# Kernel tuning notes

Hardware: AMD Instinct MI355X
Metric: run time of the kernel (lower is better)

The kernel has to match this reference:

```python
import jax, jax.numpy as jnp
import numpy as np

# Master-Slave MoE: dense shared 'master' expert Mlp applied to every token,
# plus num_experts 'slave' Mlp experts combined via top-k softmax gating,
# output = master(x) + sum_k gate_k * expert_k(x). Each Mlp: fc2(gelu(fc1(x))).

DIM = 512
HID = 4 * DIM
NUM_EXPERTS = 8
TOP_K = 2


def mlp(x, w1, b1, w2, b2):
    h = jax.nn.gelu(jnp.einsum('bnd,dh->bnh', x, w1) + b1)
    return jnp.einsum('bnh,hd->bnd', h, w2) + b2


def setup_inputs() -> dict:
    key = jax.random.key(0)
    ks = jax.random.split(key, 10)
    B, N = 4, 4096
    s1 = 1.0 / np.sqrt(DIM)
    s2 = 1.0 / np.sqrt(HID)
    return {
        'x': jax.random.normal(ks[0], (B, N, DIM), jnp.float32),
        'gate_w': jax.random.normal(ks[1], (DIM, NUM_EXPERTS), jnp.float32) * s1,
        'master_w1': jax.random.normal(ks[2], (DIM, HID), jnp.float32) * s1,
        'master_b1': jnp.zeros((HID,), jnp.float32),
        'master_w2': jax.random.normal(ks[3], (HID, DIM), jnp.float32) * s2,
        'master_b2': jnp.zeros((DIM,), jnp.float32),
        'expert_w1': jax.random.normal(ks[4], (NUM_EXPERTS, DIM, HID), jnp.float32) * s1,
        'expert_b1': jnp.zeros((NUM_EXPERTS, HID), jnp.float32),
        'expert_w2': jax.random.normal(ks[5], (NUM_EXPERTS, HID, DIM), jnp.float32) * s2,
        'expert_b2': jnp.zeros((NUM_EXPERTS, DIM), jnp.float32),
    }


def reference(x, gate_w, master_w1, master_b1, master_w2, master_b2,
              expert_w1, expert_b1, expert_w2, expert_b2):
    B, N, D = x.shape
    # Router: top-k softmax gating over experts
    logits = jnp.einsum('bnd,de->bne', x, gate_w)  # [B,N,E]
    topv, topi = jax.lax.top_k(logits, TOP_K)       # [B,N,K]
    gates_k = jax.nn.softmax(topv, axis=-1)         # [B,N,K]
    # dense gate matrix [B,N,E] (zeros for non-selected experts)
    gates = jnp.zeros_like(logits)
    gates = jnp.take_along_axis(gates, topi, axis=-1)  # noop to keep shape clarity
    gates = jnp.zeros_like(logits).at[
        jnp.arange(B)[:, None, None],
        jnp.arange(N)[None, :, None],
        topi].set(gates_k)

    # Master (shared) expert applied to all tokens
    master_out = mlp(x, master_w1, master_b1, master_w2, master_b2)

    # Slave experts: compute per-expert Mlp (vectorized over experts),
    # combine with gate weights. Gate is sparse (only top-k nonzero),
    # mathematically equal to token routing.
    h = jax.nn.gelu(jnp.einsum('bnd,edh->ebnh', x, expert_w1)
                    + expert_b1[:, None, None, :])          # [E,B,N,H]
    eo = jnp.einsum('ebnh,ehd->ebnd', h, expert_w2) \
         + expert_b2[:, None, None, :]                       # [E,B,N,D]
    slave_out = jnp.einsum('bne,ebnd->bnd', gates, eo)

    return master_out + slave_out
```

## Files before the change

### kernel.cpp

```cpp
#include <hip/hip_runtime.h>

#define DIM 512
#define HID 2048
#define NE 8

typedef _Float16 half8v __attribute__((ext_vector_type(8)));
typedef _Float16 half4v __attribute__((ext_vector_type(4)));
typedef float f32x4 __attribute__((ext_vector_type(4)));

__device__ __forceinline__ void gload16(const void* g, void* l) {
  __builtin_amdgcn_global_load_lds(
      (const __attribute__((address_space(1))) void*)g,
      (__attribute__((address_space(3))) void*)l, 16, 0, 0);
}

__global__ void k_cast_fp16(const float* __restrict__ src, _Float16* __restrict__ dst, int n4) {
  int i = blockIdx.x * blockDim.x + threadIdx.x;
  int stride = gridDim.x * blockDim.x;
  for (; i < n4; i += stride) {
    float4 v = ((const float4*)src)[i];
    half4v h = { (_Float16)v.x, (_Float16)v.y, (_Float16)v.z, (_Float16)v.w };
    ((half4v*)dst)[i] = h;
  }
}

__global__ void k_transpose_cast(const float* __restrict__ src, _Float16* __restrict__ dst,
                                 int R, int C) {
  __shared__ _Float16 ts[64][66];
  int z = blockIdx.z;
  src += (size_t)z * R * C;
  dst += (size_t)z * R * C;
  int c0 = blockIdx.x * 64, r0 = blockIdx.y * 64;
  int t = threadIdx.x;
  int rr = t >> 4, cc = (t & 15) * 4;
  #pragma unroll
  for (int i = 0; i < 4; i++) {
    int row = rr + i * 16;
    float4 v = *(const float4*)&src[(size_t)(r0 + row) * C + c0 + cc];
    ts[row][cc + 0] = (_Float16)v.x; ts[row][cc + 1] = (_Float16)v.y;
    ts[row][cc + 2] = (_Float16)v.z; ts[row][cc + 3] = (_Float16)v.w;
  }
  __syncthreads();
  int cr = t >> 4, rb = (t & 15) * 4;
  #pragma unroll
  for (int i = 0; i < 4; i++) {
    int c = cr + i * 16;
    half4v o = { ts[rb + 0][c], ts[rb + 1][c], ts[rb + 2][c], ts[rb + 3][c] };
    *(half4v*)&dst[(size_t)(c0 + c) * R + r0 + rb] = o;
  }
}

#define RT_TOK 16
__global__ void k_router(const float* __restrict__ x, const float* __restrict__ gw,
                         int* __restrict__ counts, int* __restrict__ perm,
                         float* __restrict__ pgate, int T) {
  __shared__ float xs[RT_TOK][520];
  __shared__ float gwt[8][520];
  __shared__ float lg[RT_TOK][8];
  int t = threadIdx.x;
  int tk0 = blockIdx.x * RT_TOK;
  for (int i = t; i < DIM * NE; i += 128) {
    int k = i >> 3, e = i & 7;
    gwt[e][k] = gw[i];
  }
  for (int i = t; i < RT_TOK * (DIM / 4); i += 128) {
    int row = i / (DIM / 4); int c4 = i % (DIM / 4);
    float4 v = *(const float4*)&x[(size_t)(tk0 + row) * DIM + c4 * 4];
    xs[row][c4 * 4 + 0] = v.x; xs[row][c4 * 4 + 1] = v.y;
    xs[row][c4 * 4 + 2] = v.z; xs[row][c4 * 4 + 3] = v.w;
  }
  __syncthreads();
  int tok = t >> 3, e = t & 7;
  float acc = 0.f;
  for (int k = 0; k < DIM; k += 4) {
    float4 xv = *(const float4*)&xs[tok][k];
    float4 wv = *(const float4*)&gwt[e][k];
    acc += xv.x * wv.x + xv.y * wv.y + xv.z * wv.z + xv.w * wv.w;
  }
  lg[tok][e] = acc;
  __syncthreads();
  if (t < RT_TOK) {
    float v0 = -1e30f, v1 = -1e30f; int i0 = 0, i1 = 0;
    #pragma unroll
    for (int j = 0; j < 8; j++) { float v = lg[t][j]; if (v > v0) { v0 = v; i0 = j; } }
    #pragma unroll
    for (int j = 0; j < 8; j++) { if (j == i0) continue; float v = lg[t][j]; if (v > v1) { v1 = v; i1 = j; } }
    float g0 = 1.f / (1.f + __expf(v1 - v0));
    float g1 = 1.f - g0;
    int token = tk0 + t;
    int p0 = atomicAdd(&counts[i0], 1);
    perm[i0 * T + p0] = token; pgate[i0 * T + p0] = g0;
    int p1 = atomicAdd(&counts[i1], 1);
    perm[i1 * T + p1] = token; pgate[i1 * T + p1] = g1;
  }
}

__global__ void k_offsets(const int* __restrict__ counts, int* __restrict__ offsets) {
  if (threadIdx.x == 0) {
    int s = 0;
    for (int e = 0; e < 8; e++) { offsets[e] = s; s += counts[e]; }
  }
}

template<int K, int MODE>
__global__ __launch_bounds__(256) void k_gemm(
    const _Float16* __restrict__ A,
    const _Float16* __restrict__ Bt,
    const float* __restrict__ bias,
    int bias_stride,
    const int* __restrict__ counts,
    int count_fixed,
    const int* __restrict__ offsets,
    const int* __restrict__ perm,
    const float* __restrict__ pgate,
    _Float16* __restrict__ hout,
    float* __restrict__ out,
    int T) {
  constexpr int N = (MODE == 0) ? HID : DIM;
  int e = blockIdx.z;
  int count = counts ? counts[e] : count_fixed;
  int m0 = blockIdx.x * 128;
  if (m0 >= count) return;
  int n0 = blockIdx.y * 128;
  int hbase = offsets ? offsets[e] : 0;
  const _Float16* Be = Bt + (size_t)e * N * K;
  const float* be = bias + (size_t)e * bias_stride;

  __shared__ _Float16 As[128 * 32];
  __shared__ _Float16 Bs[128 * 32];

  int t = threadIdx.x;
  int lane = t & 63;
  int wid = t >> 6;
  int wm = (wid & 1) * 64, wn = (wid >> 1) * 64;

  const char* aSrc[2]; const char* bSrc[2];
  #pragma unroll
  for (int i = 0; i < 2; i++) {
    int s = t + i * 256;
    int r = s >> 2, ch = s & 3;
    int pos = m0 + r; int pr = pos < count ? pos : count - 1;
    int arow;
    if (MODE == 0) arow = perm ? perm[e * T + pr] : pr;
    else           arow = hbase + pr;
    aSrc[i] = (const char*)(A + (size_t)arow * K) + ch * 16;
    bSrc[i] = (const char*)(Be + (size_t)(n0 + r) * K) + ch * 16;
  }

  f32x4 acc[4][4] = {};

  for (int kt = 0; kt < K / 32; ++kt) {
    gload16(aSrc[0], (char*)As + t * 16);
    gload16(aSrc[1], (char*)As + t * 16 + 4096);
    gload16(bSrc[0], (char*)Bs + t * 16);
    gload16(bSrc[1], (char*)Bs + t * 16 + 4096);
    aSrc[0] += 64; aSrc[1] += 64; bSrc[0] += 64; bSrc[1] += 64;
    __syncthreads();
    half8v af[4], bf[4];
    #pragma unroll
    for (int mi = 0; mi < 4; mi++)
      af[mi] = *(const half8v*)&As[(wm + mi * 16 + (lane & 15)) * 32 + (lane >> 4) * 8];
    #pragma unroll
    for (int ni = 0; ni < 4; ni++)
      bf[ni] = *(const half8v*)&Bs[(wn + ni * 16 + (lane & 15)) * 32 + (lane >> 4) * 8];
    #pragma unroll
    for (int mi = 0; mi < 4; mi++)
      #pragma unroll
      for (int ni = 0; ni < 4; ni++)
        acc[mi][ni] = __builtin_amdgcn_mfma_f32_16x16x32_f16(af[mi], bf[ni], acc[mi][ni], 0, 0, 0);
    __syncthreads();
  }

  int cl = lane & 15, rh = (lane >> 4) * 4;
  float bv[4];
  #pragma unroll
  for (int ni = 0; ni < 4; ni++) bv[ni] = be[n0 + wn + ni * 16 + cl];
  #pragma unroll
  for (int mi = 0; mi < 4; mi++) {
    #pragma unroll
    for (int r = 0; r < 4; r++) {
      int pos = m0 + wm + mi * 16 + rh + r;
      if (pos >= count) continue;
      int orow; float g = 1.f;
      if (MODE == 0) orow = hbase + pos;
      else {
        orow = perm ? perm[e * T + pos] : pos;
        if (MODE == 2) g = pgate[e * T + pos];
      }
      #pragma unroll
      for (int ni = 0; ni < 4; ni++) {
        float v = acc[mi][ni][r] + bv[ni];
        int col = n0 + wn + ni * 16 + cl;
        if (MODE == 0) {
          float ge = v / (1.f + __expf(-1.5957691216057308f * (v + 0.044715f * v * v * v)));
          hout[(size_t)orow * HID + col] = (_Float16)ge;
        } else if (MODE == 1) {
          out[(size_t)orow * DIM + col] = v;
        } else {
          unsafeAtomicAdd(&out[(size_t)orow * DIM + col], g * v);
        }
      }
    }
  }
}

extern "C" void kernel_launch(void* const* d_in, const int* in_sizes, int n_in,
                              void* d_out, int out_size, void* d_ws, size_t ws_size,
                              hipStream_t stream) {
  const float* x         = (const float*)d_in[0];
  const float* gate_w    = (const float*)d_in[1];
  const float* master_w1 = (const float*)d_in[2];
  const float* master_b1 = (const float*)d_in[3];
  const float* master_w2 = (const float*)d_in[4];
  const float* master_b2 = (const float*)d_in[5];
  const float* expert_w1 = (const float*)d_in[6];
  const float* expert_b1 = (const float*)d_in[7];
  const float* expert_w2 = (const float*)d_in[8];
  const float* expert_b2 = (const float*)d_in[9];
  float* out = (float*)d_out;
  int T = in_sizes[0] / DIM;

  char* p = (char*)d_ws;
  _Float16* xb   = (_Float16*)p; p += (size_t)T * DIM * 2;
  _Float16* wb1t = (_Float16*)p; p += (size_t)9 * HID * DIM * 2;
  _Float16* wb2t = (_Float16*)p; p += (size_t)9 * DIM * HID * 2;
  int*   counts  = (int*)p;      p += 256;
  int*   offsets = (int*)p;      p += 256;
  int*   perm    = (int*)p;      p += (size_t)8 * T * 4;
  float* pgate   = (float*)p;    p += (size_t)8 * T * 4;
  _Float16* hbuf = (_Float16*)p; p += (size_t)2 * T * HID * 2;

  hipMemsetAsync(counts, 0, 64, stream);

  k_cast_fp16<<<1024, 256, 0, stream>>>(x, xb, T * DIM / 4);

  k_transpose_cast<<<dim3(HID / 64, DIM / 64, 8), 256, 0, stream>>>(expert_w1, wb1t, DIM, HID);
  k_transpose_cast<<<dim3(HID / 64, DIM / 64, 1), 256, 0, stream>>>(master_w1, wb1t + (size_t)8 * HID * DIM, DIM, HID);
  k_transpose_cast<<<dim3(DIM / 64, HID / 64, 8), 256, 0, stream>>>(expert_w2, wb2t, HID, DIM);
  k_transpose_cast<<<dim3(DIM / 64, HID / 64, 1), 256, 0, stream>>>(master_w2, wb2t + (size_t)8 * DIM * HID, HID, DIM);

  k_router<<<T / RT_TOK, 128, 0, stream>>>(x, gate_w, counts, perm, pgate, T);
  k_offsets<<<1, 64, 0, stream>>>(counts, offsets);

  k_gemm<DIM, 0><<<dim3(T / 128, HID / 128, 1), 256, 0, stream>>>(
      xb, wb1t + (size_t)8 * HID * DIM, master_b1, 0, nullptr, T, nullptr, nullptr, nullptr,
      hbuf, nullptr, T);
  k_gemm<HID, 1><<<dim3(T / 128, DIM / 128, 1), 256, 0, stream>>>(
      hbuf, wb2t + (size_t)8 * DIM * HID, master_b2, 0, nullptr, T, nullptr, nullptr, nullptr,
      nullptr, out, T);

  k_gemm<DIM, 0><<<dim3(T / 128, HID / 128, 8), 256, 0, stream>>>(
      xb, wb1t, expert_b1, HID, counts, 0, offsets, perm, nullptr,
      hbuf, nullptr, T);
  k_gemm<HID, 2><<<dim3(T / 128, DIM / 128, 8), 256, 0, stream>>>(
      hbuf, wb2t, expert_b2, DIM, counts, 0, offsets, perm, pgate,
      nullptr, out, T);
}
```

Baseline: 599.0 us.

## Double-buffer LDS tiles in GEMM and XOR-swizzle layout to avoid bank conflicts

Adds a second LDS buffer for the A and B tiles so the global-to-LDS load of the next K-slice runs while the MFMAs consume the current one. Manual vmcnt waits and barriers order the stages. The 16-byte chunks in each LDS row are also XOR-swizzled, with matching reads, to cut bank conflicts on the fragment loads. This doubles LDS use per block, which could lower occupancy, and the hand-written waitcnt logic depends on exact load counts.

```diff
diff --git a/kernel.cpp b/kernel.cpp
--- a/kernel.cpp
+++ b/kernel.cpp
@@ -100,6 +100,26 @@
     int s = 0;
     for (int e = 0; e < 8; e++) { offsets[e] = s; s += counts[e]; }
   }
+}
+
+
+__device__ __forceinline__ void compute_tile(const _Float16* Asb, const _Float16* Bsb,
+                                             int wm, int wn, int lane, int rb,
+                                             f32x4 acc[4][4]) {
+  const char* ab = (const char*)Asb;
+  const char* bb = (const char*)Bsb;
+  half8v af[4], bf[4];
+  #pragma unroll
+  for (int mi = 0; mi < 4; mi++)
+    af[mi] = *(const half8v*)(ab + ((wm + mi * 16) << 6) + rb);
+  #pragma unroll
+  for (int ni = 0; ni < 4; ni++)
+    bf[ni] = *(const half8v*)(bb + ((wn + ni * 16) << 6) + rb);
+  #pragma unroll
+  for (int mi = 0; mi < 4; mi++)
+    #pragma unroll
+    for (int ni = 0; ni < 4; ni++)
+      acc[mi][ni] = __builtin_amdgcn_mfma_f32_16x16x32_f16(af[mi], bf[ni], acc[mi][ni], 0, 0, 0);
 }
 
 template<int K, int MODE>
@@ -117,6 +137,7 @@
     float* __restrict__ out,
     int T) {
   constexpr int N = (MODE == 0) ? HID : DIM;
+  constexpr int KT = K / 32;
   int e = blockIdx.z;
   int count = counts ? counts[e] : count_fixed;
   int m0 = blockIdx.x * 128;
@@ -126,50 +147,63 @@
   const _Float16* Be = Bt + (size_t)e * N * K;
   const float* be = bias + (size_t)e * bias_stride;
 
-  __shared__ _Float16 As[128 * 32];
-  __shared__ _Float16 Bs[128 * 32];
+  __shared__ _Float16 As[2][128 * 32];
+  __shared__ _Float16 Bs[2][128 * 32];
 
   int t = threadIdx.x;
   int lane = t & 63;
   int wid = t >> 6;
   int wm = (wid & 1) * 64, wn = (wid >> 1) * 64;
 
-  const char* aSrc[2]; const char* bSrc[2];
-  #pragma unroll
-  for (int i = 0; i < 2; i++) {
-    int s = t + i * 256;
-    int r = s >> 2, ch = s & 3;
-    int pos = m0 + r; int pr = pos < count ? pos : count - 1;
-    int arow;
-    if (MODE == 0) arow = perm ? perm[e * T + pr] : pr;
-    else           arow = hbase + pr;
-    aSrc[i] = (const char*)(A + (size_t)arow * K) + ch * 16;
-    bSrc[i] = (const char*)(Be + (size_t)(n0 + r) * K) + ch * 16;
-  }
+  const char* aSrc0; const char* aSrc1; const char* bSrc0; const char* bSrc1;
+  {
+    int s0 = t,        r0a = s0 >> 2, cg0 = (s0 & 3) ^ ((r0a + (r0a >> 2)) & 3);
+    int s1 = t + 256,  r1a = s1 >> 2, cg1 = (s1 & 3) ^ ((r1a + (r1a >> 2)) & 3);
+    int pos0 = m0 + r0a; int pr0 = pos0 < count ? pos0 : count - 1;
+    int pos1 = m0 + r1a; int pr1 = pos1 < count ? pos1 : count - 1;
+    int arow0, arow1;
+    if (MODE == 0) { arow0 = perm ? perm[e * T + pr0] : pr0; arow1 = perm ? perm[e * T + pr1] : pr1; }
+    else           { arow0 = hbase + pr0; arow1 = hbase + pr1; }
+    aSrc0 = (const char*)(A + (size_t)arow0 * K) + cg0 * 16;
+    aSrc1 = (const char*)(A + (size_t)arow1 * K) + cg1 * 16;
+    bSrc0 = (const char*)(Be + (size_t)(n0 + r0a) * K) + cg0 * 16;
+    bSrc1 = (const char*)(Be + (size_t)(n0 + r1a) * K) + cg1 * 16;
+  }
+
+  int cR = (lane >> 4) ^ (((lane & 3) + ((lane >> 2) & 3)) & 3);
+  int rb = ((lane & 15) << 6) + (cR << 4);
 
   f32x4 acc[4][4] = {};
 
-  for (int kt = 0; kt < K / 32; ++kt) {
-    gload16(aSrc[0], (char*)As + t * 16);
-    gload16(aSrc[1], (char*)As + t * 16 + 4096);
-    gload16(bSrc[0], (char*)Bs + t * 16);
-    gload16(bSrc[1], (char*)Bs + t * 16 + 4096);
-    aSrc[0] += 64; aSrc[1] += 64; bSrc[0] += 64; bSrc[1] += 64;
-    __syncthreads();
-    half8v af[4], bf[4];
-    #pragma unroll
-    for (int mi = 0; mi < 4; mi++)
-      af[mi] = *(const half8v*)&As[(wm + mi * 16 + (lane & 15)) * 32 + (lane >> 4) * 8];
-    #pragma unroll
-    for (int ni = 0; ni < 4; ni++)
-      bf[ni] = *(const half8v*)&Bs[(wn + ni * 16 + (lane & 15)) * 32 + (lane >> 4) * 8];
-    #pragma unroll
-    for (int mi = 0; mi < 4; mi++)
-      #pragma unroll
-      for (int ni = 0; ni < 4; ni++)
-        acc[mi][ni] = __builtin_amdgcn_mfma_f32_16x16x32_f16(af[mi], bf[ni], acc[mi][ni], 0, 0, 0);
-    __syncthreads();
-  }
+#define STAGE(buf, off) do { \
+    gload16(aSrc0 + (off), (char*)As[buf] + t * 16); \
+    gload16(aSrc1 + (off), (char*)As[buf] + t * 16 + 4096); \
+    gload16(bSrc0 + (off), (char*)Bs[buf] + t * 16); \
+    gload16(bSrc1 + (off), (char*)Bs[buf] + t * 16 + 4096); \
+  } while (0)
+
+  STAGE(0, 0);
+  for (int kt = 0; kt < KT; kt += 2) {
+    STAGE(1, (kt + 1) * 64);
+    asm volatile("s_waitcnt vmcnt(4)" ::: "memory");
+    __builtin_amdgcn_s_barrier();
+    __builtin_amdgcn_sched_barrier(0);
+    compute_tile(As[0], Bs[0], wm, wn, lane, rb, acc);
+    __builtin_amdgcn_sched_barrier(0);
+    __builtin_amdgcn_s_barrier();
+    if (kt + 2 < KT) {
+      STAGE(0, (kt + 2) * 64);
+      asm volatile("s_waitcnt vmcnt(4)" ::: "memory");
+    } else {
+      asm volatile("s_waitcnt vmcnt(0)" ::: "memory");
+    }
+    __builtin_amdgcn_s_barrier();
+    __builtin_amdgcn_sched_barrier(0);
+    compute_tile(As[1], Bs[1], wm, wn, lane, rb, acc);
+    __builtin_amdgcn_sched_barrier(0);
+    __builtin_amdgcn_s_barrier();
+  }
+#undef STAGE
 
   int cl = lane & 15, rh = (lane >> 4) * 4;
   float bv[4];
```

Result: no change. 603.4 us (+0.7%).
